# Performance work log

Measured on AMD Instinct MI355X. Metric: run time of the kernel, lower is better.

Reference implementation:

```python
import jax, jax.numpy as jnp
import numpy as np

T, B, D, L = 512, 64, 1024, 1024  # seq_len, batch, input_dim, latent_dim


def setup_inputs() -> dict:
    key = jax.random.key(0)
    ks = jax.random.split(key, 5)
    s = 1.0 / np.sqrt(D + L)  # fan-in scale for gate linears
    x = jax.random.normal(ks[0], (T, B, D), dtype=jnp.float32)
    Wf = jax.random.normal(ks[1], (D + L, L), dtype=jnp.float32) * s
    Wi = jax.random.normal(ks[2], (D + L, L), dtype=jnp.float32) * s
    Wo = jax.random.normal(ks[3], (D + L, L), dtype=jnp.float32) * s
    Wg = jax.random.normal(ks[4], (D + L, L), dtype=jnp.float32) * s
    z = jnp.zeros((L,), dtype=jnp.float32)
    return {"x": x, "Wf": Wf, "bf": z, "Wi": Wi, "bi": z,
            "Wo": Wo, "bo": z, "Wg": Wg, "bg": z}


def reference(x, Wf, bf, Wi, bi, Wo, bo, Wg, bg):
    # x: [T, B, D]; each gate W: [D+L, L]. Fuse the four gate GEMMs into one.
    L_ = Wf.shape[1]
    Wcat = jnp.concatenate([Wf, Wi, Wo, Wg], axis=1)       # [D+L, 4L]
    bcat = jnp.concatenate([bf, bi, bo, bg], axis=0)       # [4L]

    def step(carry, xt):
        h, c = carry                                        # [B, L] each
        z = jnp.concatenate([xt, h], axis=-1)               # [B, D+L]
        gates = z @ Wcat + bcat                             # [B, 4L]
        f = jax.nn.sigmoid(gates[:, 0 * L_:1 * L_])
        i = jax.nn.sigmoid(gates[:, 1 * L_:2 * L_])
        o = jax.nn.sigmoid(gates[:, 2 * L_:3 * L_])
        g = jnp.tanh(gates[:, 3 * L_:4 * L_])
        c_new = f * c + i * g
        h_new = o * jnp.tanh(c_new)
        return (h_new, c_new), h_new

    Bt = x.shape[1]
    h0 = jnp.zeros((Bt, L_), dtype=x.dtype)
    c0 = jnp.zeros((Bt, L_), dtype=x.dtype)
    _, hs = jax.lax.scan(step, (h0, c0), x)                 # hs: [T, B, L]
    return hs
```

## Files before the change

kernel.cpp:

```cpp
#include <hip/hip_runtime.h>
#include <hip/hip_bf16.h>
#include <cstdint>
#include <cstddef>

typedef short short8 __attribute__((ext_vector_type(8)));
typedef float f32x4 __attribute__((ext_vector_type(4)));
typedef int i32x4 __attribute__((ext_vector_type(4)));
typedef unsigned long long u64;
typedef unsigned int u32;

#define TT 512
#define BB 64
#define DD 1024
#define LL 1024

__global__ __launch_bounds__(256) void transpose_w(
    const float* __restrict__ Wf, const float* __restrict__ Wi,
    const float* __restrict__ Wo, const float* __restrict__ Wg,
    __hip_bfloat16* __restrict__ Wt) {
  __shared__ float tile[32][33];
  const int g = blockIdx.z;
  const float* W = (g == 0) ? Wf : (g == 1) ? Wi : (g == 2) ? Wo : Wg;
  const int k0 = blockIdx.x * 32, l0 = blockIdx.y * 32;
  const int c = threadIdx.x & 31, r0 = threadIdx.x >> 5;
#pragma unroll
  for (int rr = 0; rr < 4; ++rr) {
    const int kk = r0 + rr * 8;
    tile[kk][c] = W[(size_t)(k0 + kk) * LL + (l0 + c)];
  }
  __syncthreads();
#pragma unroll
  for (int rr = 0; rr < 4; ++rr) {
    const int ll = r0 + rr * 8;
    Wt[((size_t)(g * LL + l0 + ll) << 11) + (k0 + c)] = __float2bfloat16(tile[c][ll]);
  }
}

__global__ __launch_bounds__(256) void xconv(const float* __restrict__ x,
                                             __hip_bfloat16* __restrict__ xbf) {
  const size_t i = (size_t)blockIdx.x * 256 + threadIdx.x;
  const float4 v = ((const float4*)x)[i];
  union { __hip_bfloat16 b[4]; uint2 u; } o;
  o.b[0] = __float2bfloat16(v.x);
  o.b[1] = __float2bfloat16(v.y);
  o.b[2] = __float2bfloat16(v.z);
  o.b[3] = __float2bfloat16(v.w);
  ((uint2*)xbf)[i] = o.u;
}

__global__ __launch_bounds__(512, 2) void lstm_persist(
    const __hip_bfloat16* __restrict__ xbf, const __hip_bfloat16* __restrict__ Wt,
    const float* __restrict__ bfv, const float* __restrict__ biv,
    const float* __restrict__ bov, const float* __restrict__ bgv,
    float* __restrict__ out, __hip_bfloat16* __restrict__ hball,
    int* __restrict__ flags) {
  __shared__ float gs[64][17];
  __shared__ int ep;

  const int tid = threadIdx.x;
  const int lane = tid & 63, w = tid >> 6;
  const int quad = lane >> 4, hc = lane & 15;
  const int bt = w & 3, kp = w >> 2;
  const int bid = blockIdx.x;
  const int l0 = bid * 4;

  if (tid == 0) ep = 0;

  const int col = ((hc >> 2) << 10) + l0 + (hc & 3);
  const __hip_bfloat16* wb = Wt + ((size_t)col << 11) + (kp << 10) + quad * 8;
  short8 Bf[32];
#pragma unroll
  for (int i = 0; i < 32; ++i) Bf[i] = *(const short8*)(wb + i * 32);

  const int rowoff = (bt << 4) + hc;

  const int pb = tid >> 1, li = (tid & 1) << 1;
  const int plA = l0 + li;
  float cr0 = 0.f, cr1 = 0.f;
  float bf0 = 0, bf1 = 0, bi0 = 0, bi1 = 0, bo0 = 0, bo1 = 0, bg0 = 0, bg1 = 0;
  if (tid < 128) {
    bf0 = bfv[plA]; bf1 = bfv[plA + 1];
    bi0 = biv[plA]; bi1 = biv[plA + 1];
    bo0 = bov[plA]; bo1 = bov[plA + 1];
    bg0 = bgv[plA]; bg1 = bgv[plA + 1];
  }
  __syncthreads();

  for (int t = 0; t < TT; ++t) {
    f32x4 acc0 = {}, acc1 = {};

    if (kp == 0) {
      const __hip_bfloat16* za = xbf + ((size_t)t << 16) + ((size_t)rowoff << 10) + quad * 8;
      short8 Af[2][8];
#pragma unroll
      for (int i = 0; i < 8; ++i) Af[0][i] = *(const short8*)(za + i * 32);
#pragma unroll
      for (int g = 0; g < 4; ++g) {
        const int cur = g & 1, nxt = cur ^ 1;
        if (g < 3) {
#pragma unroll
          for (int i = 0; i < 8; ++i)
            Af[nxt][i] = *(const short8*)(za + (g + 1) * 256 + i * 32);
        }
#pragma unroll
        for (int i = 0; i < 8; ++i) {
          if (i & 1)
            acc1 = __builtin_amdgcn_mfma_f32_16x16x32_bf16(Af[cur][i], Bf[g * 8 + i], acc1, 0, 0, 0);
          else
            acc0 = __builtin_amdgcn_mfma_f32_16x16x32_bf16(Af[cur][i], Bf[g * 8 + i], acc0, 0, 0, 0);
        }
      }
    } else if (t > 0) {
      if (w == 4) {
        const int* fp4 = flags + (lane << 2);
        int ok = 0, spins = 0;
        while (!ok && spins < (1 << 16)) {
          i32x4 f;
          asm volatile("global_load_dwordx4 %0, %1, off sc0 sc1"
                       : "=v"(f) : "v"(fp4));
          asm volatile("s_waitcnt vmcnt(0)" ::: "memory");
          ok = __all((f[0] >= t) & (f[1] >= t) & (f[2] >= t) & (f[3] >= t));
          if (!ok) { __builtin_amdgcn_s_sleep(2); ++spins; }
        }
        __hip_atomic_store(&ep, t, __ATOMIC_RELAXED, __HIP_MEMORY_SCOPE_WORKGROUP);
      } else {
        int spins = 0;
        while (__hip_atomic_load(&ep, __ATOMIC_RELAXED,
                                 __HIP_MEMORY_SCOPE_WORKGROUP) < t) {
          if (++spins > (1 << 22)) break;
        }
      }
      asm volatile("" ::: "memory");

      const u64* hp = (const u64*)(hball + ((size_t)(t - 1) << 16)) + (quad << 7) + rowoff;
      union frag { short8 s; u64 u[2]; };
      frag Ah[2][8];
#pragma unroll
      for (int i = 0; i < 8; ++i) {
        Ah[0][i].u[0] = hp[i * 512];
        Ah[0][i].u[1] = hp[i * 512 + 64];
      }
#pragma unroll
      for (int g = 0; g < 4; ++g) {
        const int cur = g & 1, nxt = cur ^ 1;
        if (g < 3) {
#pragma unroll
          for (int i = 0; i < 8; ++i) {
            Ah[nxt][i].u[0] = hp[(g + 1) * 4096 + i * 512];
            Ah[nxt][i].u[1] = hp[(g + 1) * 4096 + i * 512 + 64];
          }
        }
#pragma unroll
        for (int i = 0; i < 8; ++i) {
          if (i & 1)
            acc1 = __builtin_amdgcn_mfma_f32_16x16x32_bf16(Ah[cur][i].s, Bf[g * 8 + i], acc1, 0, 0, 0);
          else
            acc0 = __builtin_amdgcn_mfma_f32_16x16x32_bf16(Ah[cur][i].s, Bf[g * 8 + i], acc0, 0, 0, 0);
        }
      }
    }

    if (kp == 1) {
#pragma unroll
      for (int r = 0; r < 4; ++r)
        gs[(bt << 4) + (quad << 2) + r][hc] = acc0[r] + acc1[r];
    }
    __syncthreads();
    if (kp == 0) {
#pragma unroll
      for (int r = 0; r < 4; ++r)
        gs[(bt << 4) + (quad << 2) + r][hc] += acc0[r] + acc1[r];
    }
    __syncthreads();

    if (tid < 128) {
      const float fp0 = gs[pb][li] + bf0,      fp1 = gs[pb][li + 1] + bf1;
      const float ip0 = gs[pb][4 + li] + bi0,  ip1 = gs[pb][5 + li] + bi1;
      const float op0 = gs[pb][8 + li] + bo0,  op1 = gs[pb][9 + li] + bo1;
      const float gp0 = gs[pb][12 + li] + bg0, gp1 = gs[pb][13 + li] + bg1;
      const float fs0 = 1.0f / (1.0f + __expf(-fp0)), fs1 = 1.0f / (1.0f + __expf(-fp1));
      const float is0 = 1.0f / (1.0f + __expf(-ip0)), is1 = 1.0f / (1.0f + __expf(-ip1));
      const float os0 = 1.0f / (1.0f + __expf(-op0)), os1 = 1.0f / (1.0f + __expf(-op1));
      const float gv0 = tanhf(gp0), gv1 = tanhf(gp1);
      cr0 = fs0 * cr0 + is0 * gv0;
      cr1 = fs1 * cr1 + is1 * gv1;
      const float h0 = os0 * tanhf(cr0), h1 = os1 * tanhf(cr1);
      float2 ov; ov.x = h0; ov.y = h1;
      *(float2*)(out + (((size_t)t) << 16) + ((size_t)pb << 10) + plA) = ov;
      union { __hip_bfloat16 b[2]; u32 uu; } hu;
      hu.b[0] = __float2bfloat16(h0);
      hu.b[1] = __float2bfloat16(h1);
      u32* hwp = (u32*)(hball + ((size_t)t << 16));
      __hip_atomic_store(hwp + (bid << 7) + tid, hu.uu,
                         __ATOMIC_RELAXED, __HIP_MEMORY_SCOPE_AGENT);
    }
    asm volatile("s_waitcnt vmcnt(0)" ::: "memory");
    __syncthreads();
    if (tid == 0)
      __hip_atomic_store(&flags[bid], t + 1, __ATOMIC_RELAXED,
                         __HIP_MEMORY_SCOPE_AGENT);
  }
}

extern "C" void kernel_launch(void* const* d_in, const int* in_sizes, int n_in,
                              void* d_out, int out_size, void* d_ws, size_t ws_size,
                              hipStream_t stream) {
  const float* x   = (const float*)d_in[0];
  const float* Wf  = (const float*)d_in[1];
  const float* bfv = (const float*)d_in[2];
  const float* Wi  = (const float*)d_in[3];
  const float* biv = (const float*)d_in[4];
  const float* Wo  = (const float*)d_in[5];
  const float* bov = (const float*)d_in[6];
  const float* Wg  = (const float*)d_in[7];
  const float* bgv = (const float*)d_in[8];
  float* out = (float*)d_out;

  __hip_bfloat16* Wt    = (__hip_bfloat16*)d_ws;
  __hip_bfloat16* xbf   = Wt + (size_t)4096 * 2048;
  __hip_bfloat16* hball = xbf + (size_t)TT * BB * LL;
  int* flags = (int*)(hball + (size_t)TT * 65536);

  transpose_w<<<dim3(64, 32, 4), 256, 0, stream>>>(Wf, Wi, Wo, Wg, Wt);
  xconv<<<dim3((TT * BB * LL) / 4 / 256), 256, 0, stream>>>(x, xbf);
  hipMemsetAsync(flags, 0, 256 * sizeof(int), stream);

  lstm_persist<<<256, 512, 0, stream>>>(xbf, Wt, bfv, biv, bov, bgv,
                                        out, hball, flags);
}
```

Baseline: 5.468 ms.

## Prefetch next-step input GEMM in separate waves and keep weights in LDS

Splits the block into two roles. Four waves compute the input projection x_{t+1}·W for the next timestep into a double-buffered shared array. The other four waves wait on the h flags, do the recurrent GEMM, add the precomputed input part and apply the gate nonlinearities locally per wave. Weights move from registers into LDS, and a __syncthreads pair per step is removed, so the critical recurrent path shrinks. The cost is LDS reads of the weights on every MFMA and a shorter spin limit.

```diff
diff --git a/kernel.cpp b/kernel.cpp
--- a/kernel.cpp
+++ b/kernel.cpp
@@ -54,146 +54,157 @@
     const float* __restrict__ bov, const float* __restrict__ bgv,
     float* __restrict__ out, __hip_bfloat16* __restrict__ hball,
     int* __restrict__ flags) {
-  __shared__ float gs[64][17];
+  __shared__ short8 wf[4096];
+  __shared__ float gw[4][16][17];
+  __shared__ float gsx[2][64][17];
   __shared__ int ep;
 
   const int tid = threadIdx.x;
   const int lane = tid & 63, w = tid >> 6;
   const int quad = lane >> 4, hc = lane & 15;
-  const int bt = w & 3, kp = w >> 2;
+  const bool isH = (w < 4);
+  const int bt = w & 3;
+  const int kp = isH ? 1 : 0;
   const int bid = blockIdx.x;
   const int l0 = bid * 4;
 
   if (tid == 0) ep = 0;
 
   const int col = ((hc >> 2) << 10) + l0 + (hc & 3);
-  const __hip_bfloat16* wb = Wt + ((size_t)col << 11) + (kp << 10) + quad * 8;
-  short8 Bf[32];
-#pragma unroll
-  for (int i = 0; i < 32; ++i) Bf[i] = *(const short8*)(wb + i * 32);
+  if (w == 0 || w == 4) {
+    const __hip_bfloat16* wb = Wt + ((size_t)col << 11) + (kp << 10) + quad * 8;
+#pragma unroll
+    for (int j = 0; j < 32; ++j)
+      wf[(kp << 11) + (j << 6) + lane] = *(const short8*)(wb + j * 32);
+  }
 
   const int rowoff = (bt << 4) + hc;
 
-  const int pb = tid >> 1, li = (tid & 1) << 1;
-  const int plA = l0 + li;
-  float cr0 = 0.f, cr1 = 0.f;
-  float bf0 = 0, bf1 = 0, bi0 = 0, bi1 = 0, bo0 = 0, bo1 = 0, bg0 = 0, bg1 = 0;
-  if (tid < 128) {
-    bf0 = bfv[plA]; bf1 = bfv[plA + 1];
-    bi0 = biv[plA]; bi1 = biv[plA + 1];
-    bo0 = bov[plA]; bo1 = bov[plA + 1];
-    bg0 = bgv[plA]; bg1 = bgv[plA + 1];
-  }
+  const int row16 = lane >> 2, lc = lane & 3;
+  const int pl = l0 + lc;
+  float cr = 0.f, bfr = 0.f, bir = 0.f, bor = 0.f, bgr = 0.f;
+  if (isH) { bfr = bfv[pl]; bir = biv[pl]; bor = bov[pl]; bgr = bgv[pl]; }
+
   __syncthreads();
 
+  auto xgemm = [&](int tt) {
+    const __hip_bfloat16* za =
+        xbf + ((size_t)tt << 16) + ((size_t)rowoff << 10) + quad * 8;
+    f32x4 a0 = {}, a1 = {};
+    short8 Af[2][8];
+#pragma unroll
+    for (int i = 0; i < 8; ++i) Af[0][i] = *(const short8*)(za + i * 32);
+#pragma unroll
+    for (int g = 0; g < 4; ++g) {
+      const int cur = g & 1, nxt = cur ^ 1;
+      if (g < 3) {
+#pragma unroll
+        for (int i = 0; i < 8; ++i)
+          Af[nxt][i] = *(const short8*)(za + (g + 1) * 256 + i * 32);
+      }
+#pragma unroll
+      for (int i = 0; i < 8; ++i) {
+        const short8 bb = wf[((g << 3) + i) * 64 + lane];
+        if (i & 1)
+          a1 = __builtin_amdgcn_mfma_f32_16x16x32_bf16(Af[cur][i], bb, a1, 0, 0, 0);
+        else
+          a0 = __builtin_amdgcn_mfma_f32_16x16x32_bf16(Af[cur][i], bb, a0, 0, 0, 0);
+      }
+    }
+    const int par = tt & 1;
+#pragma unroll
+    for (int r = 0; r < 4; ++r)
+      gsx[par][(bt << 4) + (quad << 2) + r][hc] = a0[r] + a1[r];
+  };
+
+  if (!isH) xgemm(0);
+  __syncthreads();
+
   for (int t = 0; t < TT; ++t) {
-    f32x4 acc0 = {}, acc1 = {};
-
-    if (kp == 0) {
-      const __hip_bfloat16* za = xbf + ((size_t)t << 16) + ((size_t)rowoff << 10) + quad * 8;
-      short8 Af[2][8];
-#pragma unroll
-      for (int i = 0; i < 8; ++i) Af[0][i] = *(const short8*)(za + i * 32);
-#pragma unroll
-      for (int g = 0; g < 4; ++g) {
-        const int cur = g & 1, nxt = cur ^ 1;
-        if (g < 3) {
-#pragma unroll
-          for (int i = 0; i < 8; ++i)
-            Af[nxt][i] = *(const short8*)(za + (g + 1) * 256 + i * 32);
+    if (!isH) {
+      if (t + 1 < TT) xgemm(t + 1);
+    } else {
+      f32x4 a0 = {}, a1 = {};
+      if (t > 0) {
+        if (w == 0) {
+          const int* fp4 = flags + (lane << 2);
+          int ok = 0, spins = 0;
+          while (!ok && spins < (1 << 14)) {
+            i32x4 f;
+            asm volatile("global_load_dwordx4 %0, %1, off sc0 sc1"
+                         : "=v"(f) : "v"(fp4));
+            asm volatile("s_waitcnt vmcnt(0)" ::: "memory");
+            ok = __all((f[0] >= t) & (f[1] >= t) & (f[2] >= t) & (f[3] >= t));
+            if (!ok) { __builtin_amdgcn_s_sleep(1); ++spins; }
+          }
+          __hip_atomic_store(&ep, t, __ATOMIC_RELAXED, __HIP_MEMORY_SCOPE_WORKGROUP);
+        } else {
+          int spins = 0;
+          while (__hip_atomic_load(&ep, __ATOMIC_RELAXED,
+                                   __HIP_MEMORY_SCOPE_WORKGROUP) < t) {
+            if (++spins > (1 << 22)) break;
+          }
         }
+        asm volatile("" ::: "memory");
+
+        const u64* hp = (const u64*)(hball + ((size_t)(t - 1) << 16)) +
+                        (quad << 7) + rowoff;
+        union frag { short8 s; u64 u[2]; };
+        frag Ah[2][8];
 #pragma unroll
         for (int i = 0; i < 8; ++i) {
-          if (i & 1)
-            acc1 = __builtin_amdgcn_mfma_f32_16x16x32_bf16(Af[cur][i], Bf[g * 8 + i], acc1, 0, 0, 0);
-          else
-            acc0 = __builtin_amdgcn_mfma_f32_16x16x32_bf16(Af[cur][i], Bf[g * 8 + i], acc0, 0, 0, 0);
+          Ah[0][i].u[0] = hp[i * 512];
+          Ah[0][i].u[1] = hp[i * 512 + 64];
         }
-      }
-    } else if (t > 0) {
-      if (w == 4) {
-        const int* fp4 = flags + (lane << 2);
-        int ok = 0, spins = 0;
-        while (!ok && spins < (1 << 16)) {
-          i32x4 f;
-          asm volatile("global_load_dwordx4 %0, %1, off sc0 sc1"
-                       : "=v"(f) : "v"(fp4));
-          asm volatile("s_waitcnt vmcnt(0)" ::: "memory");
-          ok = __all((f[0] >= t) & (f[1] >= t) & (f[2] >= t) & (f[3] >= t));
-          if (!ok) { __builtin_amdgcn_s_sleep(2); ++spins; }
+#pragma unroll
+        for (int g = 0; g < 4; ++g) {
+          const int cur = g & 1, nxt = cur ^ 1;
+          if (g < 3) {
+#pragma unroll
+            for (int i = 0; i < 8; ++i) {
+              Ah[nxt][i].u[0] = hp[(g + 1) * 4096 + i * 512];
+              Ah[nxt][i].u[1] = hp[(g + 1) * 4096 + i * 512 + 64];
+            }
+          }
+#pragma unroll
+          for (int i = 0; i < 8; ++i) {
+            const short8 bb = wf[2048 + ((g << 3) + i) * 64 + lane];
+            if (i & 1)
+              a1 = __builtin_amdgcn_mfma_f32_16x16x32_bf16(Ah[cur][i].s, bb, a1, 0, 0, 0);
+            else
+              a0 = __builtin_amdgcn_mfma_f32_16x16x32_bf16(Ah[cur][i].s, bb, a0, 0, 0, 0);
+          }
         }
-        __hip_atomic_store(&ep, t, __ATOMIC_RELAXED, __HIP_MEMORY_SCOPE_WORKGROUP);
-      } else {
-        int spins = 0;
-        while (__hip_atomic_load(&ep, __ATOMIC_RELAXED,
-                                 __HIP_MEMORY_SCOPE_WORKGROUP) < t) {
-          if (++spins > (1 << 22)) break;
-        }
-      }
-      asm volatile("" ::: "memory");
-
-      const u64* hp = (const u64*)(hball + ((size_t)(t - 1) << 16)) + (quad << 7) + rowoff;
-      union frag { short8 s; u64 u[2]; };
-      frag Ah[2][8];
-#pragma unroll
-      for (int i = 0; i < 8; ++i) {
-        Ah[0][i].u[0] = hp[i * 512];
-        Ah[0][i].u[1] = hp[i * 512 + 64];
-      }
-#pragma unroll
-      for (int g = 0; g < 4; ++g) {
-        const int cur = g & 1, nxt = cur ^ 1;
-        if (g < 3) {
-#pragma unroll
-          for (int i = 0; i < 8; ++i) {
-            Ah[nxt][i].u[0] = hp[(g + 1) * 4096 + i * 512];
-            Ah[nxt][i].u[1] = hp[(g + 1) * 4096 + i * 512 + 64];
-          }
-        }
-#pragma unroll
-        for (int i = 0; i < 8; ++i) {
-          if (i & 1)
-            acc1 = __builtin_amdgcn_mfma_f32_16x16x32_bf16(Ah[cur][i].s, Bf[g * 8 + i], acc1, 0, 0, 0);
-          else
-            acc0 = __builtin_amdgcn_mfma_f32_16x16x32_bf16(Ah[cur][i].s, Bf[g * 8 + i], acc0, 0, 0, 0);
-        }
+      }
+
+#pragma unroll
+      for (int r = 0; r < 4; ++r)
+        gw[bt][(quad << 2) + r][hc] =
+            a0[r] + a1[r] + gsx[t & 1][(bt << 4) + (quad << 2) + r][hc];
+
+      const float fp = gw[bt][row16][lc] + bfr;
+      const float ip = gw[bt][row16][4 + lc] + bir;
+      const float op = gw[bt][row16][8 + lc] + bor;
+      const float gp = gw[bt][row16][12 + lc] + bgr;
+      const float fs = 1.0f / (1.0f + __expf(-fp));
+      const float is = 1.0f / (1.0f + __expf(-ip));
+      const float os = 1.0f / (1.0f + __expf(-op));
+      const float gv = tanhf(gp);
+      cr = fs * cr + is * gv;
+      const float h = os * tanhf(cr);
+      const int b = (bt << 4) + row16;
+      out[((size_t)t << 16) + ((size_t)b << 10) + pl] = h;
+      const float hn = __shfl_xor(h, 1);
+      if ((lc & 1) == 0) {
+        union { __hip_bfloat16 x[2]; u32 u; } hu;
+        hu.x[0] = __float2bfloat16(h);
+        hu.x[1] = __float2bfloat16(hn);
+        u32* hwp = (u32*)(hball + ((size_t)t << 16));
+        __hip_atomic_store(hwp + (bid << 7) + (b << 1) + (lc >> 1), hu.u,
+                           __ATOMIC_RELAXED, __HIP_MEMORY_SCOPE_AGENT);
       }
     }
 
-    if (kp == 1) {
-#pragma unroll
-      for (int r = 0; r < 4; ++r)
-        gs[(bt << 4) + (quad << 2) + r][hc] = acc0[r] + acc1[r];
-    }
-    __syncthreads();
-    if (kp == 0) {
-#pragma unroll
-      for (int r = 0; r < 4; ++r)
-        gs[(bt << 4) + (quad << 2) + r][hc] += acc0[r] + acc1[r];
-    }
-    __syncthreads();
-
-    if (tid < 128) {
-      const float fp0 = gs[pb][li] + bf0,      fp1 = gs[pb][li + 1] + bf1;
-      const float ip0 = gs[pb][4 + li] + bi0,  ip1 = gs[pb][5 + li] + bi1;
-      const float op0 = gs[pb][8 + li] + bo0,  op1 = gs[pb][9 + li] + bo1;
-      const float gp0 = gs[pb][12 + li] + bg0, gp1 = gs[pb][13 + li] + bg1;
-      const float fs0 = 1.0f / (1.0f + __expf(-fp0)), fs1 = 1.0f / (1.0f + __expf(-fp1));
-      const float is0 = 1.0f / (1.0f + __expf(-ip0)), is1 = 1.0f / (1.0f + __expf(-ip1));
-      const float os0 = 1.0f / (1.0f + __expf(-op0)), os1 = 1.0f / (1.0f + __expf(-op1));
-      const float gv0 = tanhf(gp0), gv1 = tanhf(gp1);
-      cr0 = fs0 * cr0 + is0 * gv0;
-      cr1 = fs1 * cr1 + is1 * gv1;
-      const float h0 = os0 * tanhf(cr0), h1 = os1 * tanhf(cr1);
-      float2 ov; ov.x = h0; ov.y = h1;
-      *(float2*)(out + (((size_t)t) << 16) + ((size_t)pb << 10) + plA) = ov;
-      union { __hip_bfloat16 b[2]; u32 uu; } hu;
-      hu.b[0] = __float2bfloat16(h0);
-      hu.b[1] = __float2bfloat16(h1);
-      u32* hwp = (u32*)(hball + ((size_t)t << 16));
-      __hip_atomic_store(hwp + (bid << 7) + tid, hu.uu,
-                         __ATOMIC_RELAXED, __HIP_MEMORY_SCOPE_AGENT);
-    }
     asm volatile("s_waitcnt vmcnt(0)" ::: "memory");
     __syncthreads();
     if (tid == 0)
```

New measurement: 4.386 ms. 1.25x faster.
